# Performance work log

Hardware: AMD Instinct MI355X
Metric: run time of the kernel (lower is better)

Reference implementation:

```python
import jax, jax.numpy as jnp
import numpy as np

N_NODES = 100000
N_EDGES = 3200000


def sage_conv(x, src, dst, Wl, bl, Wr, n_nodes):
    # PyG SAGEConv: out = lin_l(mean_{j in N(i)} x_j) + lin_r(x_i)
    msgs = x[src]                                            # [E, d]
    agg = jax.ops.segment_sum(msgs, dst, num_segments=n_nodes)
    cnt = jax.ops.segment_sum(jnp.ones((src.shape[0],), x.dtype), dst,
                              num_segments=n_nodes)
    mean = agg / jnp.maximum(cnt, 1.0)[:, None]
    return mean @ Wl.T + bl + x @ Wr.T


def setup_inputs() -> dict:
    key = jax.random.key(0)
    ks = jax.random.split(key, 9)
    x = jax.random.normal(ks[0], (N_NODES, 6), dtype=jnp.float32)
    edge_index = jax.random.randint(ks[1], (2, N_EDGES), 0, N_NODES, dtype=jnp.int32)
    def glorot(k, shape):
        fan_in = shape[1]
        return jax.random.normal(k, shape, dtype=jnp.float32) / np.sqrt(fan_in)
    return {
        "x": x,
        "edge_index": edge_index,
        "W1l": glorot(ks[2], (12, 6)), "b1": jnp.zeros((12,), jnp.float32),
        "W1r": glorot(ks[3], (12, 6)),
        "W2l": glorot(ks[4], (24, 12)), "b2": jnp.zeros((24,), jnp.float32),
        "W2r": glorot(ks[5], (24, 12)),
        "W3l": glorot(ks[6], (6, 24)), "b3": jnp.zeros((6,), jnp.float32),
        "W3r": glorot(ks[7], (6, 24)),
    }


def reference(x, edge_index, W1l, b1, W1r, W2l, b2, W2r, W3l, b3, W3r):
    src, dst = edge_index[0], edge_index[1]
    h = jax.nn.relu(sage_conv(x, src, dst, W1l, b1, W1r, N_NODES))
    h = jax.nn.relu(sage_conv(h, src, dst, W2l, b2, W2r, N_NODES))
    z = sage_conv(h, src, dst, W3l, b3, W3r, N_NODES)          # [N, 6] encoding
    return z
```

## Files before the change

### kernel.cpp

```cpp
#include <hip/hip_runtime.h>
#include <hip/hip_fp16.h>


#define BSHIFT 9
#define BMASK  511
#define NBMAX  256
#define PART_EDGES 4096
#define BCAP   18000
#define SSTRIDE 128

#define NTL(p) __builtin_nontemporal_load(p)

__device__ __forceinline__ unsigned h2u(__half2 h) { return *reinterpret_cast<unsigned*>(&h); }
__device__ __forceinline__ __half2 u2h(unsigned u) { return *reinterpret_cast<__half2*>(&u); }

__device__ __forceinline__ __half2 red32(__half2 v) {
    int x;
    x = __builtin_amdgcn_update_dpp(0, (int)h2u(v), 0x128, 0xf, 0xf, true);
    v = __hadd2(v, u2h((unsigned)x));
    x = __builtin_amdgcn_update_dpp(0, (int)h2u(v), 0x124, 0xf, 0xf, true);
    v = __hadd2(v, u2h((unsigned)x));
    x = __builtin_amdgcn_update_dpp(0, (int)h2u(v), 0x122, 0xf, 0xf, true);
    v = __hadd2(v, u2h((unsigned)x));
    x = __builtin_amdgcn_update_dpp(0, (int)h2u(v), 0x121, 0xf, 0xf, true);
    v = __hadd2(v, u2h((unsigned)x));
    v = __hadd2(v, u2h(__shfl_xor(h2u(v), 16, 64)));
    return v;
}

__device__ __forceinline__ int wscan_incl(int x) {
    x += __builtin_amdgcn_update_dpp(0, x, 0x111, 0xf, 0xf, true);
    x += __builtin_amdgcn_update_dpp(0, x, 0x112, 0xf, 0xf, true);
    x += __builtin_amdgcn_update_dpp(0, x, 0x114, 0xf, 0xf, true);
    x += __builtin_amdgcn_update_dpp(0, x, 0x118, 0xf, 0xf, true);
    x += __builtin_amdgcn_update_dpp(0, x, 0x142, 0xa, 0xf, true);
    x += __builtin_amdgcn_update_dpp(0, x, 0x143, 0xc, 0xf, true);
    return x;
}

__global__ void __launch_bounds__(256)
partition_kernel(const float* __restrict__ x, __half* __restrict__ xh,
                 __half* __restrict__ h1, __half* __restrict__ z3lh,
                 const int* __restrict__ src, const int* __restrict__ dst,
                 int* __restrict__ bcur, unsigned* __restrict__ pairs,
                 int E, int n, int nb) {
    __shared__ int hcnt[NBMAX];
    __shared__ int hbase[NBMAX];
    __shared__ int lofs[NBMAX];
    __shared__ int wtot[4];
    __shared__ unsigned sorted[PART_EDGES];
    __shared__ int gpos[PART_EDGES];

    int t = threadIdx.x;

    int gid = blockIdx.x * 256 + t;
    if (gid <= n) {
        uint4 o = make_uint4(0u, 0u, 0u, 0u);
        if (gid < n) {
            const float2* xp = reinterpret_cast<const float2*>(x + (size_t)gid * 6);
            float2 a = xp[0], b = xp[1], c = xp[2];
            o.x = h2u(__floats2half2_rn(a.x, a.y));
            o.y = h2u(__floats2half2_rn(b.x, b.y));
            o.z = h2u(__floats2half2_rn(c.x, c.y));
        }
        *reinterpret_cast<uint4*>(xh + (size_t)gid * 8) = o;
    }
    if (blockIdx.x == 0) {
        if (t < 16) h1[(size_t)n * 16 + t] = __float2half(0.f);
        if (t < 8)  z3lh[(size_t)n * 8 + t] = __float2half(0.f);
    }

    int lo = blockIdx.x * PART_EDGES;
    int hi = min(E, lo + PART_EDGES);
    int cnt = hi - lo;

    for (int i = t; i < NBMAX; i += 256) hcnt[i] = 0;
    __syncthreads();

    int myd[16]; unsigned mys[16];
#pragma unroll
    for (int k = 0; k < 16; k++) {
        int i = lo + t + k * 256;
        if (i < hi) { myd[k] = NTL(dst + i); mys[k] = (unsigned)NTL(src + i); }
        else myd[k] = -1;
    }
#pragma unroll
    for (int k = 0; k < 16; k++)
        if (myd[k] >= 0) atomicAdd(&hcnt[myd[k] >> BSHIFT], 1);
    __syncthreads();

    int c = (t < nb) ? hcnt[t] : 0;
    if (t < nb) hbase[t] = c ? (t * BCAP + atomicAdd(&bcur[t], c)) : 0;
    int sc = wscan_incl(c);
    if ((t & 63) == 63) wtot[t >> 6] = sc;
    __syncthreads();
    int ofs = 0;
#pragma unroll
    for (int j = 0; j < 3; j++)
        if (j < (t >> 6)) ofs += wtot[j];
    int excl = sc + ofs - c;
    if (t < nb) { lofs[t] = excl; hcnt[t] = excl; }
    __syncthreads();

#pragma unroll
    for (int k = 0; k < 16; k++) {
        if (myd[k] >= 0) {
            int d = myd[k];
            int b = d >> BSHIFT;
            int r = atomicAdd(&hcnt[b], 1);
            sorted[r] = (mys[k] << BSHIFT) | (unsigned)(d & BMASK);
            gpos[r] = hbase[b] + (r - lofs[b]);
        }
    }
    __syncthreads();

    for (int i = t; i < cnt; i += 256)
        pairs[gpos[i]] = sorted[i];
}

__global__ void __launch_bounds__(1024)
csr_build(const unsigned* __restrict__ pairs,
          const int* __restrict__ bcur,
          int* __restrict__ deg,
          int* __restrict__ ssrc, int n) {
    __shared__ int lcur[512];
    int b = blockIdx.x;
    int base = b * BCAP;
    int cnt = bcur[b];
    int t = threadIdx.x;
    if (t < 512) lcur[t] = 0;
    __syncthreads();
    for (int i = t; i < cnt; i += 1024) {
        unsigned p = NTL(pairs + base + i);
        int loc = p & BMASK;
        int pos = atomicAdd(&lcur[loc], 1);
        if (pos < SSTRIDE)
            ssrc[(size_t)((b << BSHIFT) + loc) * SSTRIDE + pos] = (int)(p >> BSHIFT);
    }
    __syncthreads();
    if (t < 512) {
        int node = (b << BSHIFT) + t;
        if (node < n) deg[node] = min(lcur[t], SSTRIDE);
    }
}

__global__ void __launch_bounds__(256)
sage_layer1(const __half* __restrict__ xh,
            const int* __restrict__ deg,
            const int* __restrict__ ssrc,
            const float* __restrict__ Wl,
            const float* __restrict__ bb,
            const float* __restrict__ Wr,
            __half* __restrict__ h1, int n) {
    __shared__ __half2 sWl2[36], sWr2[36];
    __shared__ float sb[12];
    int t = threadIdx.x;
    if (t < 36) {
        int r = t / 3, k = t % 3;
        sWl2[t] = __halves2half2(__float2half(Wl[r * 6 + 2 * k]),
                                 __float2half(Wl[r * 6 + 2 * k + 1]));
        sWr2[t] = __halves2half2(__float2half(Wr[r * 6 + 2 * k]),
                                 __float2half(Wr[r * 6 + 2 * k + 1]));
    }
    if (t < 12) sb[t] = bb[t];
    __syncthreads();

    int wid = (blockIdx.x * blockDim.x + threadIdx.x) >> 6;
    int nwaves = (gridDim.x * blockDim.x) >> 6;
    int wl = threadIdx.x & 63;
    int lane = wl & 31;
    int sub = wl >> 5;

    int r = (lane < 12) ? lane : 0;
    __half2 wl2[3], wr2[3];
#pragma unroll
    for (int k = 0; k < 3; k++) { wl2[k] = sWl2[r * 3 + k]; wr2[k] = sWr2[r * 3 + k]; }
    float bias = sb[r];

    int npairs = (n + 1) >> 1;
    __half2 z2 = __float2half2_rn(0.f);

    int pA = wid, pB = wid + nwaves;
    int nodeA = 2 * pA + sub, nodeB = 2 * pB + sub;
    bool vA = (pA < npairs) && (nodeA < n);
    bool vB = (pB < npairs) && (nodeB < n);
    int offA = vA ? nodeA * SSTRIDE : 0;
    int offB = vB ? nodeB * SSTRIDE : 0;
    int dgA = vA ? deg[nodeA] : 0;
    int dgB = vB ? deg[nodeB] : 0;

    int qa0 = ssrc[offA + lane], qa1 = ssrc[offA + lane + 32];
    int qb0 = ssrc[offB + lane], qb1 = ssrc[offB + lane + 32];
    int sa0 = (lane < dgA) ? qa0 : n;
    int sa1 = (lane + 32 < dgA) ? qa1 : n;
    int sb0_ = (lane < dgB) ? qb0 : n;
    int sb1_ = (lane + 32 < dgB) ? qb1 : n;
    uint4 ra0 = *reinterpret_cast<const uint4*>(xh + (size_t)sa0 * 8);
    uint4 ra1 = *reinterpret_cast<const uint4*>(xh + (size_t)sa1 * 8);
    uint4 rb0 = *reinterpret_cast<const uint4*>(xh + (size_t)sb0_ * 8);
    uint4 rb1 = *reinterpret_cast<const uint4*>(xh + (size_t)sb1_ * 8);

    __half2 aA[3], aB[3];
    aA[0] = __hadd2(u2h(ra0.x), u2h(ra1.x));
    aA[1] = __hadd2(u2h(ra0.y), u2h(ra1.y));
    aA[2] = __hadd2(u2h(ra0.z), u2h(ra1.z));
    aB[0] = __hadd2(u2h(rb0.x), u2h(rb1.x));
    aB[1] = __hadd2(u2h(rb0.y), u2h(rb1.y));
    aB[2] = __hadd2(u2h(rb0.z), u2h(rb1.z));

    int m = max(dgA, dgB);
    for (int e = lane + 64; e < m; e += 32) {
        int qa = ssrc[offA + e];
        int qb = ssrc[offB + e];
        int sa = (e < dgA) ? qa : n;
        int sbx = (e < dgB) ? qb : n;
        uint4 ta = *reinterpret_cast<const uint4*>(xh + (size_t)sa * 8);
        uint4 tb = *reinterpret_cast<const uint4*>(xh + (size_t)sbx * 8);
        aA[0] = __hadd2(aA[0], u2h(ta.x)); aA[1] = __hadd2(aA[1], u2h(ta.y));
        aA[2] = __hadd2(aA[2], u2h(ta.z));
        aB[0] = __hadd2(aB[0], u2h(tb.x)); aB[1] = __hadd2(aB[1], u2h(tb.y));
        aB[2] = __hadd2(aB[2], u2h(tb.z));
    }

#pragma unroll
    for (int k = 0; k < 3; k++) { aA[k] = red32(aA[k]); aB[k] = red32(aB[k]); }

    auto epi = [&](int node, int dg, __half2* acc, bool valid) {
        if (valid && lane < 12) {
            uint4 xr = *reinterpret_cast<const uint4*>(xh + (size_t)node * 8);
            __half2 xi2[3] = { u2h(xr.x), u2h(xr.y), u2h(xr.z) };
            __half2 S1 = z2, S2 = z2;
#pragma unroll
            for (int k = 0; k < 3; k++) {
                S1 = __hfma2(acc[k], wl2[k], S1);
                S2 = __hfma2(xi2[k], wr2[k], S2);
            }
            float inv = 1.f / (float)(dg > 0 ? dg : 1);
            float o = (__low2float(S1) + __high2float(S1)) * inv
                    + __low2float(S2) + __high2float(S2) + bias;
            h1[(size_t)node * 16 + lane] = __float2half(fmaxf(o, 0.f));
        }
    };
    epi(nodeA, dgA, aA, vA);
    epi(nodeB, dgB, aB, vB);
}

__global__ void __launch_bounds__(256)
sage_layer2(const __half* __restrict__ h1,
            const int* __restrict__ deg,
            const int* __restrict__ ssrc,
            const float* __restrict__ W2l,
            const float* __restrict__ b2,
            const float* __restrict__ W2r,
            const float* __restrict__ W3l,
            const float* __restrict__ W3r,
            __half* __restrict__ z3lh,
            float* __restrict__ z3r, int n) {
    __shared__ __half2 sW2l2[144], sW2r2[144];
    __shared__ float sW3[300], sb2[24];
    __shared__ __attribute__((aligned(16))) float sh2[4][48];
    int t = threadIdx.x;
    if (t < 144) {
        int r = t / 6, k = t % 6;
        sW2l2[t] = __halves2half2(__float2half(W2l[r * 12 + 2 * k]),
                                  __float2half(W2l[r * 12 + 2 * k + 1]));
        sW2r2[t] = __halves2half2(__float2half(W2r[r * 12 + 2 * k]),
                                  __float2half(W2r[r * 12 + 2 * k + 1]));
        int r3 = t / 24, c3 = t % 24;
        sW3[r3 * 25 + c3] = W3l[t];
        sW3[(r3 + 6) * 25 + c3] = W3r[t];
    }
    if (t < 24) sb2[t] = b2[t];
    __syncthreads();

    int wid = (blockIdx.x * blockDim.x + threadIdx.x) >> 6;
    int nwaves = (gridDim.x * blockDim.x) >> 6;
    int wv = threadIdx.x >> 6;
    int wl = threadIdx.x & 63;
    int lane = wl & 31;
    int sub = wl >> 5;

    int r2 = (lane < 24) ? lane : 0;
    __half2 w2l2[6], w2r2[6];
#pragma unroll
    for (int k = 0; k < 6; k++) { w2l2[k] = sW2l2[r2 * 6 + k]; w2r2[k] = sW2r2[r2 * 6 + k]; }
    float bias = sb2[r2];
    int w3off = (lane < 12) ? lane * 25 : 0;

    int npairs = (n + 1) >> 1;
    __half2 z2 = __float2half2_rn(0.f);

    int p0 = wid, p1 = wid + nwaves;
    int node0 = 2 * p0 + sub, node1 = 2 * p1 + sub;
    bool v0 = (p0 < npairs) && (node0 < n);
    bool v1 = (p1 < npairs) && (node1 < n);
    int off0 = v0 ? node0 * SSTRIDE : 0;
    int off1 = v1 ? node1 * SSTRIDE : 0;
    int dg0 = v0 ? deg[node0] : 0;
    int dg1 = v1 ? deg[node1] : 0;

    int qa0 = ssrc[off0 + lane], qa1 = ssrc[off0 + lane + 32];
    int qb0 = ssrc[off1 + lane], qb1 = ssrc[off1 + lane + 32];
    int sa0 = (lane < dg0) ? qa0 : n;
    int sa1 = (lane + 32 < dg0) ? qa1 : n;
    int sb0_ = (lane < dg1) ? qb0 : n;
    int sb1_ = (lane + 32 < dg1) ? qb1 : n;
    const char* pa0 = reinterpret_cast<const char*>(h1 + (size_t)sa0 * 16);
    const char* pa1 = reinterpret_cast<const char*>(h1 + (size_t)sa1 * 16);
    const char* pb0 = reinterpret_cast<const char*>(h1 + (size_t)sb0_ * 16);
    const char* pb1 = reinterpret_cast<const char*>(h1 + (size_t)sb1_ * 16);
    uint4 Aa0 = *reinterpret_cast<const uint4*>(pa0);
    uint2 Ba0 = *reinterpret_cast<const uint2*>(pa0 + 16);
    uint4 Aa1 = *reinterpret_cast<const uint4*>(pa1);
    uint2 Ba1 = *reinterpret_cast<const uint2*>(pa1 + 16);
    uint4 Ab0 = *reinterpret_cast<const uint4*>(pb0);
    uint2 Bb0 = *reinterpret_cast<const uint2*>(pb0 + 16);
    uint4 Ab1 = *reinterpret_cast<const uint4*>(pb1);
    uint2 Bb1 = *reinterpret_cast<const uint2*>(pb1 + 16);

    __half2 a0[6], a1[6];
    a0[0] = __hadd2(u2h(Aa0.x), u2h(Aa1.x)); a0[1] = __hadd2(u2h(Aa0.y), u2h(Aa1.y));
    a0[2] = __hadd2(u2h(Aa0.z), u2h(Aa1.z)); a0[3] = __hadd2(u2h(Aa0.w), u2h(Aa1.w));
    a0[4] = __hadd2(u2h(Ba0.x), u2h(Ba1.x)); a0[5] = __hadd2(u2h(Ba0.y), u2h(Ba1.y));
    a1[0] = __hadd2(u2h(Ab0.x), u2h(Ab1.x)); a1[1] = __hadd2(u2h(Ab0.y), u2h(Ab1.y));
    a1[2] = __hadd2(u2h(Ab0.z), u2h(Ab1.z)); a1[3] = __hadd2(u2h(Ab0.w), u2h(Ab1.w));
    a1[4] = __hadd2(u2h(Bb0.x), u2h(Bb1.x)); a1[5] = __hadd2(u2h(Bb0.y), u2h(Bb1.y));

    int m = max(dg0, dg1);
    for (int e = lane + 64; e < m; e += 32) {
        int qa = ssrc[off0 + e];
        int qb = ssrc[off1 + e];
        int sa = (e < dg0) ? qa : n;
        int sbx = (e < dg1) ? qb : n;
        const char* ta = reinterpret_cast<const char*>(h1 + (size_t)sa * 16);
        const char* tb = reinterpret_cast<const char*>(h1 + (size_t)sbx * 16);
        uint4 Ta = *reinterpret_cast<const uint4*>(ta);
        uint2 Ua = *reinterpret_cast<const uint2*>(ta + 16);
        uint4 Tb = *reinterpret_cast<const uint4*>(tb);
        uint2 Ub = *reinterpret_cast<const uint2*>(tb + 16);
        a0[0] = __hadd2(a0[0], u2h(Ta.x)); a0[1] = __hadd2(a0[1], u2h(Ta.y));
        a0[2] = __hadd2(a0[2], u2h(Ta.z)); a0[3] = __hadd2(a0[3], u2h(Ta.w));
        a0[4] = __hadd2(a0[4], u2h(Ua.x)); a0[5] = __hadd2(a0[5], u2h(Ua.y));
        a1[0] = __hadd2(a1[0], u2h(Tb.x)); a1[1] = __hadd2(a1[1], u2h(Tb.y));
        a1[2] = __hadd2(a1[2], u2h(Tb.z)); a1[3] = __hadd2(a1[3], u2h(Tb.w));
        a1[4] = __hadd2(a1[4], u2h(Ub.x)); a1[5] = __hadd2(a1[5], u2h(Ub.y));
    }

    auto finish = [&](int node, int dg, __half2* acc, bool valid) {
#pragma unroll
        for (int k = 0; k < 6; k++) acc[k] = red32(acc[k]);

        float h2v = 0.f;
        if (valid && lane < 24) {
            const char* rp = reinterpret_cast<const char*>(h1 + (size_t)node * 16);
            uint4 x0 = *reinterpret_cast<const uint4*>(rp);
            uint2 x1 = *reinterpret_cast<const uint2*>(rp + 16);
            __half2 xi2[6] = { u2h(x0.x), u2h(x0.y), u2h(x0.z),
                               u2h(x0.w), u2h(x1.x), u2h(x1.y) };
            __half2 S1 = z2, S2 = z2;
#pragma unroll
            for (int k = 0; k < 6; k++) {
                S1 = __hfma2(acc[k], w2l2[k], S1);
                S2 = __hfma2(xi2[k], w2r2[k], S2);
            }
            float inv = 1.f / (float)(dg > 0 ? dg : 1);
            float o = (__low2float(S1) + __high2float(S1)) * inv
                    + __low2float(S2) + __high2float(S2) + bias;
            h2v = fmaxf(o, 0.f);
        }
        if (lane < 24) sh2[wv][sub * 24 + lane] = h2v;
        float z = 0.f;
        if (lane < 12) {
            const float4* hp = reinterpret_cast<const float4*>(sh2[wv] + sub * 24);
#pragma unroll
            for (int k = 0; k < 6; k++) {
                float4 h4 = hp[k];
                float w0 = sW3[w3off + 4 * k],     w1 = sW3[w3off + 4 * k + 1];
                float w2 = sW3[w3off + 4 * k + 2], w3 = sW3[w3off + 4 * k + 3];
                z += h4.x * w0 + h4.y * w1 + h4.z * w2 + h4.w * w3;
            }
        }
        if (valid) {
            if (lane < 6)               z3lh[(size_t)node * 8 + lane] = __float2half(z);
            else if (lane < 8)          z3lh[(size_t)node * 8 + lane] = __float2half(0.f);
            if (lane >= 6 && lane < 12) z3r[(size_t)node * 6 + (lane - 6)] = z;
        }
    };
    finish(node0, dg0, a0, v0);
    finish(node1, dg1, a1, v1);
}

__global__ void __launch_bounds__(256)
sage_layer3(const __half* __restrict__ z3lh,
            const int* __restrict__ deg,
            const int* __restrict__ ssrc,
            const float* __restrict__ b3,
            const float* __restrict__ z3r,
            float* __restrict__ out, int n) {
    int wid = (blockIdx.x * blockDim.x + threadIdx.x) >> 6;
    int nwaves = (gridDim.x * blockDim.x) >> 6;
    int wl = threadIdx.x & 63;
    int lane = wl & 31;
    int sub = wl >> 5;

    float b3v = b3[(lane < 6) ? lane : 0];

    int npairs = (n + 1) >> 1;

    int pA = wid, pB = wid + nwaves;
    int nodeA = 2 * pA + sub, nodeB = 2 * pB + sub;
    bool vA = (pA < npairs) && (nodeA < n);
    bool vB = (pB < npairs) && (nodeB < n);
    int offA = vA ? nodeA * SSTRIDE : 0;
    int offB = vB ? nodeB * SSTRIDE : 0;
    int dgA = vA ? deg[nodeA] : 0;
    int dgB = vB ? deg[nodeB] : 0;

    int qa0 = ssrc[offA + lane], qa1 = ssrc[offA + lane + 32];
    int qb0 = ssrc[offB + lane], qb1 = ssrc[offB + lane + 32];
    int sa0 = (lane < dgA) ? qa0 : n;
    int sa1 = (lane + 32 < dgA) ? qa1 : n;
    int sb0_ = (lane < dgB) ? qb0 : n;
    int sb1_ = (lane + 32 < dgB) ? qb1 : n;
    uint4 ra0 = *reinterpret_cast<const uint4*>(z3lh + (size_t)sa0 * 8);
    uint4 ra1 = *reinterpret_cast<const uint4*>(z3lh + (size_t)sa1 * 8);
    uint4 rb0 = *reinterpret_cast<const uint4*>(z3lh + (size_t)sb0_ * 8);
    uint4 rb1 = *reinterpret_cast<const uint4*>(z3lh + (size_t)sb1_ * 8);

    __half2 aA[3], aB[3];
    aA[0] = __hadd2(u2h(ra0.x), u2h(ra1.x));
    aA[1] = __hadd2(u2h(ra0.y), u2h(ra1.y));
    aA[2] = __hadd2(u2h(ra0.z), u2h(ra1.z));
    aB[0] = __hadd2(u2h(rb0.x), u2h(rb1.x));
    aB[1] = __hadd2(u2h(rb0.y), u2h(rb1.y));
    aB[2] = __hadd2(u2h(rb0.z), u2h(rb1.z));

    int m = max(dgA, dgB);
    for (int e = lane + 64; e < m; e += 32) {
        int qa = ssrc[offA + e];
        int qb = ssrc[offB + e];
        int sa = (e < dgA) ? qa : n;
        int sbx = (e < dgB) ? qb : n;
        uint4 ta = *reinterpret_cast<const uint4*>(z3lh + (size_t)sa * 8);
        uint4 tb = *reinterpret_cast<const uint4*>(z3lh + (size_t)sbx * 8);
        aA[0] = __hadd2(aA[0], u2h(ta.x)); aA[1] = __hadd2(aA[1], u2h(ta.y));
        aA[2] = __hadd2(aA[2], u2h(ta.z));
        aB[0] = __hadd2(aB[0], u2h(tb.x)); aB[1] = __hadd2(aB[1], u2h(tb.y));
        aB[2] = __hadd2(aB[2], u2h(tb.z));
    }

#pragma unroll
    for (int k = 0; k < 3; k++) { aA[k] = red32(aA[k]); aB[k] = red32(aB[k]); }

    auto epi = [&](int node, int dg, __half2* acc, bool valid) {
        if (valid && lane < 6) {
            float fa[6] = { __low2float(acc[0]), __high2float(acc[0]),
                            __low2float(acc[1]), __high2float(acc[1]),
                            __low2float(acc[2]), __high2float(acc[2]) };
            float inv = 1.f / (float)(dg > 0 ? dg : 1);
            out[(size_t)node * 6 + lane] = fa[lane] * inv + b3v
                                         + z3r[(size_t)node * 6 + lane];
        }
    };
    epi(nodeA, dgA, aA, vA);
    epi(nodeB, dgB, aB, vB);
}

extern "C" void kernel_launch(void* const* d_in, const int* in_sizes, int n_in,
                              void* d_out, int out_size, void* d_ws, size_t ws_size,
                              hipStream_t stream) {
    const float* x   = (const float*)d_in[0];
    const int* eidx  = (const int*)d_in[1];
    const float* W1l = (const float*)d_in[2];
    const float* b1  = (const float*)d_in[3];
    const float* W1r = (const float*)d_in[4];
    const float* W2l = (const float*)d_in[5];
    const float* b2  = (const float*)d_in[6];
    const float* W2r = (const float*)d_in[7];
    const float* W3l = (const float*)d_in[8];
    const float* b3  = (const float*)d_in[9];
    const float* W3r = (const float*)d_in[10];

    const int n = in_sizes[0] / 6;
    const int E = in_sizes[1] / 2;
    const int* src = eidx;
    const int* dst = eidx + E;
    const int nb = (n + BMASK) >> BSHIFT;

    char* w = (char*)d_ws;
    auto carve = [&](size_t bytes) {
        char* p = w;
        w += (bytes + 255) & ~(size_t)255;
        return p;
    };
    int*      bcur    = (int*)carve((size_t)NBMAX * 4);
    unsigned* pairs   = (unsigned*)carve((size_t)nb * BCAP * 4);
    int*      ssrc    = (int*)carve((size_t)(nb << BSHIFT) * SSTRIDE * 4 + 256);
    int*      deg     = (int*)carve((size_t)n * 4);
    __half*   xh      = (__half*)carve((size_t)(n + 1) * 8 * 2);
    __half*   h1      = (__half*)carve((size_t)(n + 1) * 16 * 2);
    __half*   z3lh    = (__half*)carve((size_t)(n + 1) * 8 * 2);
    float*    z3r     = (float*)carve((size_t)n * 6 * 4);

    const int part_blocks = (E + PART_EDGES - 1) / PART_EDGES;

    hipMemsetAsync(bcur, 0, (size_t)NBMAX * 4, stream);
    partition_kernel<<<part_blocks, 256, 0, stream>>>(x, xh, h1, z3lh,
                                                      src, dst, bcur, pairs, E, n, nb);
    csr_build<<<nb, 1024, 0, stream>>>(pairs, bcur, deg, ssrc, n);

    const int LBLK = 6250;
    sage_layer1<<<LBLK, 256, 0, stream>>>(xh, deg, ssrc, W1l, b1, W1r, h1, n);
    sage_layer2<<<LBLK, 256, 0, stream>>>(h1, deg, ssrc,
                                          W2l, b2, W2r, W3l, W3r, z3lh, z3r, n);
    sage_layer3<<<LBLK, 256, 0, stream>>>(z3lh, deg, ssrc, b3, z3r,
                                          (float*)d_out, n);
}
```

Before: 204.5 us.

## Fuse CSR bucket build with layer-1 aggregation in one kernel

Merges the per-bucket CSR construction kernel and the layer-1 SAGE kernel into a single kernel. Each 1024-thread block builds the adjacency slots for its 512 destination nodes, keeps the degrees in shared memory, and then its 32-lane half-waves aggregate and transform those same nodes. This removes one launch and the global reread of deg, and may let the freshly written ssrc rows be read back from cache. The cost is that layer-1 work now runs on only nb (about 196) blocks instead of 6250, so there is far less parallelism to hide the latency of the random gathers.

```diff
diff --git a/kernel.cpp b/kernel.cpp
--- a/kernel.cpp
+++ b/kernel.cpp
@@ -119,39 +119,16 @@
 }
 
 __global__ void __launch_bounds__(1024)
-csr_build(const unsigned* __restrict__ pairs,
-          const int* __restrict__ bcur,
-          int* __restrict__ deg,
-          int* __restrict__ ssrc, int n) {
+csr_layer1(const unsigned* __restrict__ pairs,
+           const int* __restrict__ bcur,
+           const __half* __restrict__ xh,
+           const float* __restrict__ Wl,
+           const float* __restrict__ bb,
+           const float* __restrict__ Wr,
+           int* __restrict__ deg,
+           int* __restrict__ ssrc,
+           __half* __restrict__ h1, int n) {
     __shared__ int lcur[512];
-    int b = blockIdx.x;
-    int base = b * BCAP;
-    int cnt = bcur[b];
-    int t = threadIdx.x;
-    if (t < 512) lcur[t] = 0;
-    __syncthreads();
-    for (int i = t; i < cnt; i += 1024) {
-        unsigned p = NTL(pairs + base + i);
-        int loc = p & BMASK;
-        int pos = atomicAdd(&lcur[loc], 1);
-        if (pos < SSTRIDE)
-            ssrc[(size_t)((b << BSHIFT) + loc) * SSTRIDE + pos] = (int)(p >> BSHIFT);
-    }
-    __syncthreads();
-    if (t < 512) {
-        int node = (b << BSHIFT) + t;
-        if (node < n) deg[node] = min(lcur[t], SSTRIDE);
-    }
-}
-
-__global__ void __launch_bounds__(256)
-sage_layer1(const __half* __restrict__ xh,
-            const int* __restrict__ deg,
-            const int* __restrict__ ssrc,
-            const float* __restrict__ Wl,
-            const float* __restrict__ bb,
-            const float* __restrict__ Wr,
-            __half* __restrict__ h1, int n) {
     __shared__ __half2 sWl2[36], sWr2[36];
     __shared__ float sb[12];
     int t = threadIdx.x;
@@ -163,76 +140,74 @@
                                  __float2half(Wr[r * 6 + 2 * k + 1]));
     }
     if (t < 12) sb[t] = bb[t];
-    __syncthreads();
-
-    int wid = (blockIdx.x * blockDim.x + threadIdx.x) >> 6;
-    int nwaves = (gridDim.x * blockDim.x) >> 6;
-    int wl = threadIdx.x & 63;
-    int lane = wl & 31;
-    int sub = wl >> 5;
-
+    if (t < 512) lcur[t] = 0;
+    __syncthreads();
+
+    int b = blockIdx.x;
+    int base = b * BCAP;
+    int cnt = bcur[b];
+
+    for (int i = t; i < cnt; i += 1024) {
+        unsigned p = NTL(pairs + base + i);
+        int loc = p & BMASK;
+        int pos = atomicAdd(&lcur[loc], 1);
+        if (pos < SSTRIDE)
+            ssrc[(size_t)((b << BSHIFT) + loc) * SSTRIDE + pos] = (int)(p >> BSHIFT);
+    }
+    __syncthreads();
+
+    if (t < 512) {
+        int node = (b << BSHIFT) + t;
+        int dgc = min(lcur[t], SSTRIDE);
+        lcur[t] = dgc;
+        if (node < n) deg[node] = dgc;
+    }
+    __syncthreads();
+
+    int hw = t >> 5;
+    int lane = t & 31;
     int r = (lane < 12) ? lane : 0;
     __half2 wl2[3], wr2[3];
 #pragma unroll
     for (int k = 0; k < 3; k++) { wl2[k] = sWl2[r * 3 + k]; wr2[k] = sWr2[r * 3 + k]; }
     float bias = sb[r];
-
-    int npairs = (n + 1) >> 1;
     __half2 z2 = __float2half2_rn(0.f);
 
-    int pA = wid, pB = wid + nwaves;
-    int nodeA = 2 * pA + sub, nodeB = 2 * pB + sub;
-    bool vA = (pA < npairs) && (nodeA < n);
-    bool vB = (pB < npairs) && (nodeB < n);
-    int offA = vA ? nodeA * SSTRIDE : 0;
-    int offB = vB ? nodeB * SSTRIDE : 0;
-    int dgA = vA ? deg[nodeA] : 0;
-    int dgB = vB ? deg[nodeB] : 0;
-
-    int qa0 = ssrc[offA + lane], qa1 = ssrc[offA + lane + 32];
-    int qb0 = ssrc[offB + lane], qb1 = ssrc[offB + lane + 32];
-    int sa0 = (lane < dgA) ? qa0 : n;
-    int sa1 = (lane + 32 < dgA) ? qa1 : n;
-    int sb0_ = (lane < dgB) ? qb0 : n;
-    int sb1_ = (lane + 32 < dgB) ? qb1 : n;
-    uint4 ra0 = *reinterpret_cast<const uint4*>(xh + (size_t)sa0 * 8);
-    uint4 ra1 = *reinterpret_cast<const uint4*>(xh + (size_t)sa1 * 8);
-    uint4 rb0 = *reinterpret_cast<const uint4*>(xh + (size_t)sb0_ * 8);
-    uint4 rb1 = *reinterpret_cast<const uint4*>(xh + (size_t)sb1_ * 8);
-
-    __half2 aA[3], aB[3];
-    aA[0] = __hadd2(u2h(ra0.x), u2h(ra1.x));
-    aA[1] = __hadd2(u2h(ra0.y), u2h(ra1.y));
-    aA[2] = __hadd2(u2h(ra0.z), u2h(ra1.z));
-    aB[0] = __hadd2(u2h(rb0.x), u2h(rb1.x));
-    aB[1] = __hadd2(u2h(rb0.y), u2h(rb1.y));
-    aB[2] = __hadd2(u2h(rb0.z), u2h(rb1.z));
-
-    int m = max(dgA, dgB);
-    for (int e = lane + 64; e < m; e += 32) {
-        int qa = ssrc[offA + e];
-        int qb = ssrc[offB + e];
-        int sa = (e < dgA) ? qa : n;
-        int sbx = (e < dgB) ? qb : n;
-        uint4 ta = *reinterpret_cast<const uint4*>(xh + (size_t)sa * 8);
-        uint4 tb = *reinterpret_cast<const uint4*>(xh + (size_t)sbx * 8);
-        aA[0] = __hadd2(aA[0], u2h(ta.x)); aA[1] = __hadd2(aA[1], u2h(ta.y));
-        aA[2] = __hadd2(aA[2], u2h(ta.z));
-        aB[0] = __hadd2(aB[0], u2h(tb.x)); aB[1] = __hadd2(aB[1], u2h(tb.y));
-        aB[2] = __hadd2(aB[2], u2h(tb.z));
-    }
-
-#pragma unroll
-    for (int k = 0; k < 3; k++) { aA[k] = red32(aA[k]); aB[k] = red32(aB[k]); }
-
-    auto epi = [&](int node, int dg, __half2* acc, bool valid) {
-        if (valid && lane < 12) {
+    for (int nl = hw; nl < 512; nl += 32) {
+        int node = (b << BSHIFT) + nl;
+        if (node >= n) continue;
+        int dg = lcur[nl];
+        int off = node * SSTRIDE;
+
+        int q0 = ssrc[off + lane], q1 = ssrc[off + lane + 32];
+        int s0 = (lane < dg) ? q0 : n;
+        int s1 = (lane + 32 < dg) ? q1 : n;
+        uint4 r0 = *reinterpret_cast<const uint4*>(xh + (size_t)s0 * 8);
+        uint4 r1 = *reinterpret_cast<const uint4*>(xh + (size_t)s1 * 8);
+
+        __half2 a[3];
+        a[0] = __hadd2(u2h(r0.x), u2h(r1.x));
+        a[1] = __hadd2(u2h(r0.y), u2h(r1.y));
+        a[2] = __hadd2(u2h(r0.z), u2h(r1.z));
+
+        for (int e = lane + 64; e < dg; e += 32) {
+            int q = ssrc[off + e];
+            uint4 tv = *reinterpret_cast<const uint4*>(xh + (size_t)q * 8);
+            a[0] = __hadd2(a[0], u2h(tv.x));
+            a[1] = __hadd2(a[1], u2h(tv.y));
+            a[2] = __hadd2(a[2], u2h(tv.z));
+        }
+
+#pragma unroll
+        for (int k = 0; k < 3; k++) a[k] = red32(a[k]);
+
+        if (lane < 12) {
             uint4 xr = *reinterpret_cast<const uint4*>(xh + (size_t)node * 8);
             __half2 xi2[3] = { u2h(xr.x), u2h(xr.y), u2h(xr.z) };
             __half2 S1 = z2, S2 = z2;
 #pragma unroll
             for (int k = 0; k < 3; k++) {
-                S1 = __hfma2(acc[k], wl2[k], S1);
+                S1 = __hfma2(a[k], wl2[k], S1);
                 S2 = __hfma2(xi2[k], wr2[k], S2);
             }
             float inv = 1.f / (float)(dg > 0 ? dg : 1);
@@ -240,9 +215,7 @@
                     + __low2float(S2) + __high2float(S2) + bias;
             h1[(size_t)node * 16 + lane] = __float2half(fmaxf(o, 0.f));
         }
-    };
-    epi(nodeA, dgA, aA, vA);
-    epi(nodeB, dgB, aB, vB);
+    }
 }
 
 __global__ void __launch_bounds__(256)
@@ -507,10 +480,10 @@
     hipMemsetAsync(bcur, 0, (size_t)NBMAX * 4, stream);
     partition_kernel<<<part_blocks, 256, 0, stream>>>(x, xh, h1, z3lh,
                                                       src, dst, bcur, pairs, E, n, nb);
-    csr_build<<<nb, 1024, 0, stream>>>(pairs, bcur, deg, ssrc, n);
+    csr_layer1<<<nb, 1024, 0, stream>>>(pairs, bcur, xh, W1l, b1, W1r,
+                                        deg, ssrc, h1, n);
 
     const int LBLK = 6250;
-    sage_layer1<<<LBLK, 256, 0, stream>>>(xh, deg, ssrc, W1l, b1, W1r, h1, n);
     sage_layer2<<<LBLK, 256, 0, stream>>>(h1, deg, ssrc,
                                           W2l, b2, W2r, W3l, W3r, z3lh, z3r, n);
     sage_layer3<<<LBLK, 256, 0, stream>>>(z3lh, deg, ssrc, b3, z3r,
```

Measured after the change: 208.9 us. 1.02x slower.
